# Kernel tuning notes

Measured on AMD Instinct MI355X. Metric: run time of the kernel, lower is better.

The kernel has to match this reference:

```python
import jax, jax.numpy as jnp
import numpy as np

# Config matching init_kwargs
K_H, K_W = 2, 2
S_H, S_W = 2, 2
EXP, MAN = 5, 10  # fp16-like custom float format
B, C, H, W = 32, 256, 112, 112
OH = (H - K_H) // S_H + 1  # 56
OW = (W - K_W) // S_W + 1  # 56
DIVISOR = K_H * K_W


def float_quantize(x, exp_bits=EXP, man_bits=MAN):
    """Round-to-nearest-even quantization to a float format with `exp_bits`
    exponent bits and `man_bits` mantissa bits (saturating, with subnormals)."""
    max_e = 2 ** (exp_bits - 1) - 1          # max IEEE exponent
    min_e = 1 - max_e                        # min normal IEEE exponent
    m, e = jnp.frexp(x)                      # x = m * 2^e, m in [0.5, 1)
    # IEEE exponent of x is (e - 1); clamp below for subnormal handling.
    step_e = jnp.maximum(e - 1, min_e) - man_bits
    scale = jnp.exp2(step_e.astype(x.dtype))
    q = jnp.round(x / scale) * scale         # round half-to-even == IEEE nearest
    max_val = jnp.asarray((2.0 - 2.0 ** (-man_bits)) * 2.0 ** max_e, x.dtype)
    return jnp.clip(q, -max_val, max_val)


def setup_inputs() -> dict:
    key = jax.random.key(0)
    x = jax.random.normal(key, (B, C, H, W), dtype=jnp.float32)
    return {"x": x}


def reference(x) -> jnp.ndarray:
    # Quantized avg-pool: y is accumulated one kernel tap at a time, with a
    # float_quantize after every add (same order as the original m,n loops).
    # The original h,w loops are independent per output pixel -> vectorized
    # here via strided slices covering all (h, w) at once.
    y = jnp.zeros((B, C, OH, OW), dtype=x.dtype)
    for m in range(K_H):
        for n in range(K_W):
            patch = x[:, :, m:m + S_H * OH:S_H, n:n + S_W * OW:S_W]  # [B,C,OH,OW]
            y = float_quantize(y + patch)
    y = float_quantize(y / DIVISOR)
    return y
```

## Files before the change

kernel.cpp:

```cpp
#include <hip/hip_runtime.h>
#include <hip/hip_fp16.h>


constexpr int B  = 32, C = 256, H = 112, W = 112;
constexpr int OH = 56, OW = 56;
constexpr int HW   = H * W;
constexpr int OHOW = OH * OW;
constexpr int NOUT = B * C * OH * OW;
constexpr int PW   = OW / 2;
constexpr int RP   = OH / 2;

typedef float vfloat4 __attribute__((ext_vector_type(4)));
typedef float vfloat2 __attribute__((ext_vector_type(2)));

__device__ __forceinline__ float q16(float v) {
    return __half2float(__float2half(v));
}

__device__ __forceinline__ float pool4(float x00, float x01, float x10, float x11) {
    float acc = q16(x00);
    acc = q16(acc + x01);
    acc = q16(acc + x10);
    acc = q16(acc + x11);
    return q16(acc * 0.25f);
}

__global__ __launch_bounds__(256)
void qavgpool2d_kernel(const float* __restrict__ x, float* __restrict__ y) {
    int t = blockIdx.x * blockDim.x + threadIdx.x;

    int pw  = t % PW;
    int tmp = t / PW;
    int r2  = tmp % RP;
    int bc  = tmp / RP;

    const float* xb = x + (size_t)bc * HW + (r2 * 4) * W + pw * 4;

    vfloat4 a0 = __builtin_nontemporal_load(reinterpret_cast<const vfloat4*>(xb));
    vfloat4 a1 = __builtin_nontemporal_load(reinterpret_cast<const vfloat4*>(xb + W));
    vfloat4 a2 = __builtin_nontemporal_load(reinterpret_cast<const vfloat4*>(xb + 2 * W));
    vfloat4 a3 = __builtin_nontemporal_load(reinterpret_cast<const vfloat4*>(xb + 3 * W));

    vfloat2 o0, o1;
    o0.x = pool4(a0.x, a0.y, a1.x, a1.y);
    o0.y = pool4(a0.z, a0.w, a1.z, a1.w);
    o1.x = pool4(a2.x, a2.y, a3.x, a3.y);
    o1.y = pool4(a2.z, a2.w, a3.z, a3.w);

    float* yb = y + (size_t)bc * OHOW + (r2 * 2) * OW + pw * 2;
    __builtin_nontemporal_store(o0, reinterpret_cast<vfloat2*>(yb));
    __builtin_nontemporal_store(o1, reinterpret_cast<vfloat2*>(yb + OW));
}

extern "C" void kernel_launch(void* const* d_in, const int* in_sizes, int n_in,
                              void* d_out, int out_size, void* d_ws, size_t ws_size,
                              hipStream_t stream) {
    const float* x = (const float*)d_in[0];
    float*       y = (float*)d_out;

    constexpr int threads = 256;
    constexpr int nthreads_total = NOUT / 4;
    constexpr int blocks = nthreads_total / threads;

    qavgpool2d_kernel<<<blocks, threads, 0, stream>>>(x, y);
}
```

Baseline: 87.71 us.

## Process eight input rows per thread and pair lanes for 16-byte stores

Each thread now loads eight input rows instead of four and produces four output rows, halving the thread count. Adjacent lanes swap half their results with a lane shuffle, so each thread writes two full 16-byte vectors instead of 8-byte ones. The aim is wider, more coalesced stores and less per-thread index overhead in this bandwidth-bound kernel. The cost is more registers per thread, fewer threads in flight to hide latency, and a correctness dependency on lane pairs sharing the same row group.

```diff
diff --git a/kernel.cpp b/kernel.cpp
--- a/kernel.cpp
+++ b/kernel.cpp
@@ -8,7 +8,7 @@
 constexpr int OHOW = OH * OW;
 constexpr int NOUT = B * C * OH * OW;
 constexpr int PW   = OW / 2;
-constexpr int RP   = OH / 2;
+constexpr int R8   = OH / 4;
 
 typedef float vfloat4 __attribute__((ext_vector_type(4)));
 typedef float vfloat2 __attribute__((ext_vector_type(2)));
@@ -31,25 +31,39 @@
 
     int pw  = t % PW;
     int tmp = t / PW;
-    int r2  = tmp % RP;
-    int bc  = tmp / RP;
+    int r8  = tmp % R8;
+    int bc  = tmp / R8;
 
-    const float* xb = x + (size_t)bc * HW + (r2 * 4) * W + pw * 4;
+    const float* xb = x + (size_t)bc * HW + (r8 * 8) * W + pw * 4;
 
-    vfloat4 a0 = __builtin_nontemporal_load(reinterpret_cast<const vfloat4*>(xb));
-    vfloat4 a1 = __builtin_nontemporal_load(reinterpret_cast<const vfloat4*>(xb + W));
-    vfloat4 a2 = __builtin_nontemporal_load(reinterpret_cast<const vfloat4*>(xb + 2 * W));
-    vfloat4 a3 = __builtin_nontemporal_load(reinterpret_cast<const vfloat4*>(xb + 3 * W));
+    vfloat4 a[8];
+    #pragma unroll
+    for (int k = 0; k < 8; ++k)
+        a[k] = __builtin_nontemporal_load(reinterpret_cast<const vfloat4*>(xb + (size_t)k * W));
 
-    vfloat2 o0, o1;
-    o0.x = pool4(a0.x, a0.y, a1.x, a1.y);
-    o0.y = pool4(a0.z, a0.w, a1.z, a1.w);
-    o1.x = pool4(a2.x, a2.y, a3.x, a3.y);
-    o1.y = pool4(a2.z, a2.w, a3.z, a3.w);
+    vfloat2 o[4];
+    #pragma unroll
+    for (int r = 0; r < 4; ++r) {
+        o[r].x = pool4(a[2*r].x, a[2*r].y, a[2*r+1].x, a[2*r+1].y);
+        o[r].y = pool4(a[2*r].z, a[2*r].w, a[2*r+1].z, a[2*r+1].w);
+    }
 
-    float* yb = y + (size_t)bc * OHOW + (r2 * 2) * OW + pw * 2;
-    __builtin_nontemporal_store(o0, reinterpret_cast<vfloat2*>(yb));
-    __builtin_nontemporal_store(o1, reinterpret_cast<vfloat2*>(yb + OW));
+    const bool odd = (threadIdx.x & 1);
+    vfloat2 s0 = odd ? o[0] : o[1];
+    vfloat2 r0; r0.x = __shfl_xor(s0.x, 1, 64); r0.y = __shfl_xor(s0.y, 1, 64);
+    vfloat2 s1 = odd ? o[2] : o[3];
+    vfloat2 r1; r1.x = __shfl_xor(s1.x, 1, 64); r1.y = __shfl_xor(s1.y, 1, 64);
+
+    vfloat4 st0, st1;
+    if (odd) { st0 = vfloat4{r0.x, r0.y, o[1].x, o[1].y};
+               st1 = vfloat4{r1.x, r1.y, o[3].x, o[3].y}; }
+    else     { st0 = vfloat4{o[0].x, o[0].y, r0.x, r0.y};
+               st1 = vfloat4{o[2].x, o[2].y, r1.x, r1.y}; }
+
+    int row = r8 * 4 + (odd ? 1 : 0);
+    float* yb = y + (size_t)bc * OHOW + row * OW + (pw & ~1) * 2;
+    __builtin_nontemporal_store(st0, reinterpret_cast<vfloat4*>(yb));
+    __builtin_nontemporal_store(st1, reinterpret_cast<vfloat4*>(yb + 2 * OW));
 }
 
 extern "C" void kernel_launch(void* const* d_in, const int* in_sizes, int n_in,
@@ -59,7 +73,7 @@
     float*       y = (float*)d_out;
 
     constexpr int threads = 256;
-    constexpr int nthreads_total = NOUT / 4;
+    constexpr int nthreads_total = NOUT / 8;
     constexpr int blocks = nthreads_total / threads;
 
     qavgpool2d_kernel<<<blocks, threads, 0, stream>>>(x, y);
```

After: 91.77 us. 4.6% more time.
